# Performance work log

Hardware: AMD Instinct MI355X
Metric: run time of the kernel (lower is better)

## Reference

```python
import jax, jax.numpy as jnp
from jax import lax
import numpy as np

EPS = 1e-5
NEG_SLOPE = 0.2

# 4D conv via lax.conv_general_dilated (supports arbitrary spatial rank)
_DN = ('NCABXY', 'OIABXY', 'NCABXY')  # N,C + 4 spatial dims

def conv4d(x, w):
    # x: (N, Cin, S1, S2, H, W); w: (Cout, Cin, 3, 3, 3, 3); padding=1, stride=1
    return lax.conv_general_dilated(
        x, w,
        window_strides=(1, 1, 1, 1),
        padding=[(1, 1)] * 4,
        dimension_numbers=_DN,
    )

def instance_norm4d(x):
    # normalize per (n, c) over all 4 spatial dims; no affine (PyTorch default)
    mean = jnp.mean(x, axis=(2, 3, 4, 5), keepdims=True)
    var = jnp.var(x, axis=(2, 3, 4, 5), keepdims=True)
    return (x - mean) * lax.rsqrt(var + EPS)

def leaky_relu(x):
    return jnp.where(x >= 0, x, NEG_SLOPE * x)

def setup_inputs() -> dict:
    key = jax.random.key(0)
    k0, k1, k2 = jax.random.split(key, 3)
    image = jax.random.normal(k0, (1, 16, 8, 16, 64, 64), dtype=jnp.float32)
    # He-ish init scale for kernel 3^4
    w1 = jax.random.normal(k1, (32, 16, 3, 3, 3, 3), dtype=jnp.float32) * 0.03
    w2 = jax.random.normal(k2, (32, 32, 3, 3, 3, 3), dtype=jnp.float32) * 0.02
    return {"image": image, "w1": w1, "w2": w2}

def reference(image, w1, w2):
    x = leaky_relu(instance_norm4d(conv4d(image, w1)))
    x = leaky_relu(instance_norm4d(conv4d(x, w2)))
    return x
```

## Files before the change

### kernel.cpp

```cpp
#include <hip/hip_runtime.h>

#define D1 8
#define D2 16
#define HH 64
#define WW 64
#define SPATIAL (D1*D2*HH*WW)
#define EPS 1e-5f
#define NEG 0.2f

typedef unsigned short u16;
typedef __attribute__((ext_vector_type(8))) short s16x8;
typedef __attribute__((ext_vector_type(8))) unsigned short u16x8;
typedef __attribute__((ext_vector_type(4))) unsigned short u16x4;
typedef __attribute__((ext_vector_type(4))) float f32x4;

__device__ __forceinline__ u16 f2bf(float f) {
    unsigned int u = __builtin_bit_cast(unsigned int, f);
    return (u16)((u + 0x7FFFu + ((u >> 16) & 1u)) >> 16);
}
__device__ __forceinline__ float bf2f(u16 u) {
    unsigned int v = ((unsigned int)u) << 16;
    return __builtin_bit_cast(float, v);
}
__device__ __forceinline__ float leaky(float x) {
    return x >= 0.f ? x : NEG * x;
}

__device__ __forceinline__ void decode_block(int flat, int& a, int& b, int& h0) {
    int xcd  = flat & 7;
    int slot = flat >> 3;
    int ht   = slot & 7;
    int b0   = (slot >> 3) & 1;
    a        = (slot >> 4) & 7;
    b        = xcd * 2 + b0;
    h0       = ht * 8;
}

__global__ __launch_bounds__(256)
void prep(const float* __restrict__ img, const float* __restrict__ w1,
          const float* __restrict__ w2, u16* __restrict__ imgT,
          u16* __restrict__ w1t, u16* __restrict__ w2t, float* __restrict__ st)
{
    const int bid = blockIdx.x;
    const int tid = threadIdx.x;
    if (bid < 2048) {
        int p = bid * 256 + tid;
        u16 r[16];
        #pragma unroll
        for (int c = 0; c < 16; ++c)
            r[c] = f2bf(img[(size_t)c * SPATIAL + p]);
        u16x8 lo, hi;
        #pragma unroll
        for (int j = 0; j < 8; ++j) { lo[j] = r[j]; hi[j] = r[8 + j]; }
        u16x8* dst = (u16x8*)(imgT + (size_t)p * 16);
        dst[0] = lo;
        dst[1] = hi;
    } else if (bid < 2264) {
        int i = (bid - 2048) * 256 + tid;
        if (i >= 55296) return;
        int k    = i & 31;
        int co   = (i >> 5) & 31;
        int grp  = (i >> 10) & 1;
        int rest = i >> 11;
        int dh   = rest % 3;
        int p    = rest / 3;
        int da = p / 3, db = p % 3;
        float v = 0.f;
        if (grp == 0) {
            int dw = k >> 4, ci = k & 15;
            v = w1[((((co * 16 + ci) * 3 + da) * 3 + db) * 3 + dh) * 3 + dw];
        } else if (k < 16) {
            v = w1[((((co * 16 + k) * 3 + da) * 3 + db) * 3 + dh) * 3 + 2];
        }
        w1t[i] = f2bf(v);
    } else if (bid < 2588) {
        int i = (bid - 2264) * 256 + tid;
        if (i >= 82944) return;
        int ci = i & 31;
        int co = (i >> 5) & 31;
        int t  = (i >> 10) % 9;
        int p  = (i >> 10) / 9;
        int da = p / 3, db = p % 3, dh = t / 3, dw = t % 3;
        w2t[i] = f2bf(w2[((((co * 32 + ci) * 3 + da) * 3 + db) * 3 + dh) * 3 + dw]);
    } else {
        if (tid < 128) st[tid] = 0.f;
    }
}

#define C1_LDBF(DST, BASE, GRP) { \
    _Pragma("unroll") \
    for (int dh_ = 0; dh_ < 3; ++dh_) { \
        const u16* wb_ = (BASE) + (dh_ * 2 + (GRP)) * 1024; \
        DST[dh_][0] = *(const s16x8*)(wb_ + m * 32 + kq * 8); \
        DST[dh_][1] = *(const s16x8*)(wb_ + (m + 16) * 32 + kq * 8); \
    } }

#define C1_MFMA(BF, CSHIFT) { \
    const int eb_ = (kq & 1) * 8; \
    _Pragma("unroll") \
    for (int x_ = 0; x_ < 10; ++x_) { \
        int pos_ = x_ * 66 + wseg + m + (CSHIFT); \
        s16x8 af_ = *(const s16x8*)&lds[pos_ * 24 + eb_]; \
        _Pragma("unroll") \
        for (int dh_ = 0; dh_ < 3; ++dh_) { \
            int i_ = x_ - dh_; \
            if (i_ >= 0 && i_ < 8) { \
                acc[i_][0] = __builtin_amdgcn_mfma_f32_16x16x32_bf16(af_, BF[dh_][0], acc[i_][0], 0, 0, 0); \
                acc[i_][1] = __builtin_amdgcn_mfma_f32_16x16x32_bf16(af_, BF[dh_][1], acc[i_][1], 0, 0, 0); \
            } \
        } \
    } }

#define C1_PF(K0, K1) { \
    _Pragma("unroll") \
    for (int k_ = (K0); k_ < (K1); ++k_) \
        if ((vmask >> k_) & 1) pf[k_] = *(const u16x8*)(srcn + gbase + k_ * 2048); }

__global__ __launch_bounds__(256, 3)
void conv1_mfma(const u16* __restrict__ xT, const u16* __restrict__ w1t,
                u16* __restrict__ y1, float* __restrict__ st1)
{
    __shared__ __align__(16) u16 lds[660 * 24];
    __shared__ float sred[64];

    const int tid = threadIdx.x;
    int a, b, h0;
    decode_block(blockIdx.x, a, b, h0);
    const int lane = tid & 63;
    const int wv   = tid >> 6;
    const int kq   = lane >> 4;
    const int m    = lane & 15;
    const int wseg = wv << 4;

    unsigned pm = 0;
    #pragma unroll
    for (int p = 0; p < 9; ++p) {
        int ap = a + p / 3 - 1, bp = b + p % 3 - 1;
        if (ap >= 0 && ap < D1 && bp >= 0 && bp < D2) pm |= 1u << p;
    }

    const int p0f  = tid >> 1, g = tid & 1;
    const int hi   = p0f >> 6;
    const int p0c  = p0f & 63;
    unsigned vmask = 0;
    #pragma unroll
    for (int k = 0; k < 5; ++k) {
        int h = h0 - 1 + 2 * k + hi;
        if (h >= 0 && h < HH) vmask |= 1u << k;
    }
    const int gbase = ((h0 - 1 + hi) * WW + p0c) * 16 + g * 8;
    const int lbase = (hi * 66 + p0c + 1) * 24 + g * 8;

    for (int e = tid; e < 660; e += 256) {
        int row = e / 66, col = e - row * 66;
        int h = h0 - 1 + row;
        if (col == 0 || col == 65 || h < 0 || h >= HH) {
            u16x8 z = (u16x8)0;
            *(u16x8*)&lds[e * 24]     = z;
            *(u16x8*)&lds[e * 24 + 8] = z;
        }
    }

    f32x4 acc[8][2];
    #pragma unroll
    for (int i = 0; i < 8; ++i)
        #pragma unroll
        for (int nt = 0; nt < 2; ++nt)
            acc[i][nt] = (f32x4)0.f;

    int p = 0;
    while (!((pm >> p) & 1)) ++p;

    s16x8 bfX[3][2], bfY[3][2];
    C1_LDBF(bfX, w1t + p * 6144, 0);

    u16x8 pf[5];
    {
        const u16* srcn = xT + (size_t)((a + p / 3 - 1) * D2 + (b + p % 3 - 1))
                             * (HH * WW * 16);
        C1_PF(0, 5);
    }

    while (p < 9) {
        int pn = p + 1;
        while (pn < 9 && !((pm >> pn) & 1)) ++pn;

        #pragma unroll
        for (int k = 0; k < 5; ++k)
            if ((vmask >> k) & 1) *(u16x8*)&lds[lbase + k * 3168] = pf[k];
        __syncthreads();

        const u16* srcn = nullptr;
        if (pn < 9)
            srcn = xT + (size_t)((a + pn / 3 - 1) * D2 + (b + pn % 3 - 1))
                      * (HH * WW * 16);

        const u16* wbase = w1t + p * 6144;

        C1_LDBF(bfY, wbase, 1);
        C1_MFMA(bfX, (kq >> 1));
        if (pn < 9) C1_PF(0, 3);

        C1_MFMA(bfY, 2);
        if (pn < 9) C1_PF(3, 5);

        __syncthreads();
        if (pn < 9) C1_LDBF(bfX, w1t + pn * 6144, 0);
        p = pn;
    }

    if (tid < 64) sred[tid] = 0.f;
    __syncthreads();

    float s[2] = {0.f, 0.f}, s2[2] = {0.f, 0.f};
    const size_t plane_out = (size_t)(a * D2 + b) * (HH * WW);
    #pragma unroll
    for (int i = 0; i < 8; ++i) {
        int h  = h0 + i;
        int w0 = wseg + kq * 4;
        #pragma unroll
        for (int nt = 0; nt < 2; ++nt) {
            int co = m + nt * 16;
            #pragma unroll
            for (int reg = 0; reg < 4; ++reg) {
                float v = acc[i][nt][reg];
                s[nt]  += v;
                s2[nt] += v * v;
                y1[(plane_out + h * WW + (w0 + reg)) * 32 + co] = f2bf(v);
            }
        }
    }
    #pragma unroll
    for (int nt = 0; nt < 2; ++nt) {
        s[nt]  += __shfl_xor(s[nt], 16);  s[nt]  += __shfl_xor(s[nt], 32);
        s2[nt] += __shfl_xor(s2[nt], 16); s2[nt] += __shfl_xor(s2[nt], 32);
    }
    if (kq == 0) {
        atomicAdd(&sred[m * 2],            s[0]);
        atomicAdd(&sred[m * 2 + 1],        s2[0]);
        atomicAdd(&sred[(m + 16) * 2],     s[1]);
        atomicAdd(&sred[(m + 16) * 2 + 1], s2[1]);
    }
    __syncthreads();
    if (tid < 64) atomicAdd(&st1[tid], sred[tid]);
}

__global__ __launch_bounds__(256)
void norm1_kernel(u16* __restrict__ y1, const float* __restrict__ st1)
{
    const int tid = threadIdx.x;
    const int q   = tid & 3;
    const float invN = 1.f / (float)SPATIAL;
    float mean[8], scl[8];
    #pragma unroll
    for (int j = 0; j < 8; ++j) {
        int ci  = q * 8 + j;
        float mu = st1[ci * 2] * invN;
        float va = st1[ci * 2 + 1] * invN - mu * mu;
        mean[j] = mu;
        scl[j]  = rsqrtf(va + EPS);
    }
    #pragma unroll
    for (int j4 = 0; j4 < 4; ++j4) {
        size_t gidx = (size_t)blockIdx.x * 1024 + j4 * 256 + tid;
        u16x8* ptr = (u16x8*)(y1 + gidx * 8);
        u16x8 v = *ptr;
        u16x8 o;
        #pragma unroll
        for (int j = 0; j < 8; ++j)
            o[j] = f2bf(leaky((bf2f(v[j]) - mean[j]) * scl[j]));
        *ptr = o;
    }
}

#define C2_LDBF(DST, BASE, DW) { \
    _Pragma("unroll") \
    for (int dh_ = 0; dh_ < 3; ++dh_) { \
        const u16* wb_ = (BASE) + (dh_ * 3 + (DW)) * 1024; \
        DST[dh_][0] = *(const s16x8*)(wb_ + m * 32 + kq * 8); \
        DST[dh_][1] = *(const s16x8*)(wb_ + (m + 16) * 32 + kq * 8); \
    } }

#define C2_MFMA(BF, DW) { \
    _Pragma("unroll") \
    for (int x_ = 0; x_ < 10; ++x_) { \
        int pos_ = x_ * 66 + wseg + (DW) + m; \
        s16x8 af_ = *(const s16x8*)&lds[pos_ * 40 + kq * 8]; \
        _Pragma("unroll") \
        for (int dh_ = 0; dh_ < 3; ++dh_) { \
            int i_ = x_ - dh_; \
            if (i_ >= 0 && i_ < 8) { \
                acc[i_][0] = __builtin_amdgcn_mfma_f32_16x16x32_bf16(af_, BF[dh_][0], acc[i_][0], 0, 0, 0); \
                acc[i_][1] = __builtin_amdgcn_mfma_f32_16x16x32_bf16(af_, BF[dh_][1], acc[i_][1], 0, 0, 0); \
            } \
        } \
    } }

#define C2_PF(K0, K1) { \
    _Pragma("unroll") \
    for (int k_ = (K0); k_ < (K1); ++k_) \
        if ((vmask >> k_) & 1) pf[k_] = *(const u16x8*)(srcn + gbase + k_ * 2048); }

__global__ __launch_bounds__(256, 3)
void conv2_mfma(const u16* __restrict__ y1, const u16* __restrict__ w2t,
                u16* __restrict__ y2, float* __restrict__ st2)
{
    __shared__ __align__(16) u16 lds[660 * 40];
    __shared__ float sred[64];

    const int tid = threadIdx.x;
    int a, b, h0;
    decode_block(blockIdx.x, a, b, h0);
    const int lane = tid & 63;
    const int wv   = tid >> 6;
    const int kq   = lane >> 4;
    const int m    = lane & 15;
    const int wseg = wv << 4;

    unsigned pm = 0;
    #pragma unroll
    for (int p = 0; p < 9; ++p) {
        int ap = a + p / 3 - 1, bp = b + p % 3 - 1;
        if (ap >= 0 && ap < D1 && bp >= 0 && bp < D2) pm |= 1u << p;
    }

    const int p0 = tid >> 2, q = tid & 3;
    unsigned vmask = 0;
    #pragma unroll
    for (int k = 0; k < 10; ++k) {
        int h = h0 - 1 + k;
        if (h >= 0 && h < HH) vmask |= 1u << k;
    }
    const int gbase = ((h0 - 1) * WW + p0) * 32 + q * 8;
    const int lbase = (p0 + 1) * 40 + q * 8;

    for (int e = tid; e < 660; e += 256) {
        int row = e / 66, col = e - row * 66;
        int h = h0 - 1 + row;
        if (col == 0 || col == 65 || h < 0 || h >= HH) {
            u16x8 z = (u16x8)0;
            #pragma unroll
            for (int gg = 0; gg < 4; ++gg)
                *(u16x8*)&lds[e * 40 + gg * 8] = z;
        }
    }

    f32x4 acc[8][2];
    #pragma unroll
    for (int i = 0; i < 8; ++i)
        #pragma unroll
        for (int nt = 0; nt < 2; ++nt)
            acc[i][nt] = (f32x4)0.f;

    int p = 0;
    while (!((pm >> p) & 1)) ++p;

    s16x8 bfX[3][2], bfY[3][2];
    C2_LDBF(bfX, w2t + p * 9216, 0);

    u16x8 pf[10];
    {
        const u16* srcn = y1 + (size_t)((a + p / 3 - 1) * D2 + (b + p % 3 - 1))
                             * (HH * WW * 32);
        C2_PF(0, 10);
    }

    while (p < 9) {
        int pn = p + 1;
        while (pn < 9 && !((pm >> pn) & 1)) ++pn;

        #pragma unroll
        for (int k = 0; k < 10; ++k)
            if ((vmask >> k) & 1) *(u16x8*)&lds[lbase + k * 2640] = pf[k];
        __syncthreads();

        const u16* srcn = nullptr;
        if (pn < 9)
            srcn = y1 + (size_t)((a + pn / 3 - 1) * D2 + (b + pn % 3 - 1))
                      * (HH * WW * 32);

        const u16* wbase = w2t + p * 9216;

        C2_LDBF(bfY, wbase, 1);
        C2_MFMA(bfX, 0);
        if (pn < 9) C2_PF(0, 4);

        C2_LDBF(bfX, wbase, 2);
        C2_MFMA(bfY, 1);
        if (pn < 9) C2_PF(4, 7);

        C2_MFMA(bfX, 2);
        if (pn < 9) C2_PF(7, 10);

        __syncthreads();
        if (pn < 9) C2_LDBF(bfX, w2t + pn * 9216, 0);
        p = pn;
    }

    if (tid < 64) sred[tid] = 0.f;
    __syncthreads();

    float s[2] = {0.f, 0.f}, s2[2] = {0.f, 0.f};
    #pragma unroll
    for (int i = 0; i < 8; ++i) {
        int h  = h0 + i;
        int w0 = wseg + kq * 4;
        #pragma unroll
        for (int nt = 0; nt < 2; ++nt) {
            int co = m + nt * 16;
            u16x4 pk;
            #pragma unroll
            for (int reg = 0; reg < 4; ++reg) {
                float v = acc[i][nt][reg];
                s[nt]  += v;
                s2[nt] += v * v;
                pk[reg] = f2bf(v);
            }
            size_t off = ((size_t)(co * D1 + a) * D2 + b) * (HH * WW) + h * WW + w0;
            *(u16x4*)(y2 + off) = pk;
        }
    }
    #pragma unroll
    for (int nt = 0; nt < 2; ++nt) {
        s[nt]  += __shfl_xor(s[nt], 16);  s[nt]  += __shfl_xor(s[nt], 32);
        s2[nt] += __shfl_xor(s2[nt], 16); s2[nt] += __shfl_xor(s2[nt], 32);
    }
    if (kq == 0) {
        atomicAdd(&sred[m * 2],            s[0]);
        atomicAdd(&sred[m * 2 + 1],        s2[0]);
        atomicAdd(&sred[(m + 16) * 2],     s[1]);
        atomicAdd(&sred[(m + 16) * 2 + 1], s2[1]);
    }
    __syncthreads();
    if (tid < 64) atomicAdd(&st2[tid], sred[tid]);
}

__global__ __launch_bounds__(256)
void norm2_kernel(const u16* __restrict__ y2, const float* __restrict__ st2,
                  float* __restrict__ out)
{
    size_t i8 = (size_t)blockIdx.x * 256 + threadIdx.x;
    int c = (int)(i8 >> 16);
    const float invN = 1.f / (float)SPATIAL;
    float mu = st2[c * 2] * invN;
    float va = st2[c * 2 + 1] * invN - mu * mu;
    float sc = rsqrtf(va + EPS);
    u16x8 v = *(const u16x8*)(y2 + i8 * 8);
    float4 o0, o1;
    o0.x = leaky((bf2f(v[0]) - mu) * sc);
    o0.y = leaky((bf2f(v[1]) - mu) * sc);
    o0.z = leaky((bf2f(v[2]) - mu) * sc);
    o0.w = leaky((bf2f(v[3]) - mu) * sc);
    o1.x = leaky((bf2f(v[4]) - mu) * sc);
    o1.y = leaky((bf2f(v[5]) - mu) * sc);
    o1.z = leaky((bf2f(v[6]) - mu) * sc);
    o1.w = leaky((bf2f(v[7]) - mu) * sc);
    float4* dst = (float4*)(out + i8 * 8);
    dst[0] = o0;
    dst[1] = o1;
}

extern "C" void kernel_launch(void* const* d_in, const int* in_sizes, int n_in,
                              void* d_out, int out_size, void* d_ws, size_t ws_size,
                              hipStream_t stream)
{
    const float* image = (const float*)d_in[0];
    const float* w1    = (const float*)d_in[1];
    const float* w2    = (const float*)d_in[2];
    float* out = (float*)d_out;

    u16*   imgT = (u16*)d_ws;
    u16*   y1   = (u16*)((char*)d_ws + 33554432);
    u16*   y2   = imgT;
    float* st   = (float*)((char*)d_ws + 67108864);
    float* st1  = st;
    float* st2  = st + 64;

    u16* w1t = (u16*)((char*)d_out + 66832384);
    u16* w2t = (u16*)((char*)d_out + 66942976);

    prep<<<2589, 256, 0, stream>>>(image, w1, w2, imgT, w1t, w2t, st);

    conv1_mfma<<<1024, 256, 0, stream>>>(imgT, w1t, y1, st1);
    norm1_kernel<<<2048, 256, 0, stream>>>(y1, st1);
    conv2_mfma<<<1024, 256, 0, stream>>>(y1, w2t, y2, st2);
    norm2_kernel<<<8192, 256, 0, stream>>>(y2, st2, out);
}
```

Before: 249.9 us.

## Split output channels across waves with 512-thread conv blocks

Both conv kernels now launch 512 threads per block. The 8 waves are split into 4 width segments times 2 output-channel halves, so each wave accumulates a single 16-channel tile instead of two. This halves per-thread accumulator, weight-fragment and prefetch registers, and the global-to-LDS staging work is spread over twice as many threads. The intent is more resident waves per CU to hide latency. The cost is that every A fragment is now read from LDS by two waves, which doubles LDS read traffic, and each block synchronizes more threads.

```diff
diff --git a/kernel.cpp b/kernel.cpp
--- a/kernel.cpp
+++ b/kernel.cpp
@@ -91,8 +91,7 @@
     _Pragma("unroll") \
     for (int dh_ = 0; dh_ < 3; ++dh_) { \
         const u16* wb_ = (BASE) + (dh_ * 2 + (GRP)) * 1024; \
-        DST[dh_][0] = *(const s16x8*)(wb_ + m * 32 + kq * 8); \
-        DST[dh_][1] = *(const s16x8*)(wb_ + (m + 16) * 32 + kq * 8); \
+        DST[dh_] = *(const s16x8*)(wb_ + cow * 32 + kq * 8); \
     } }
 
 #define C1_MFMA(BF, CSHIFT) { \
@@ -104,19 +103,17 @@
         _Pragma("unroll") \
         for (int dh_ = 0; dh_ < 3; ++dh_) { \
             int i_ = x_ - dh_; \
-            if (i_ >= 0 && i_ < 8) { \
-                acc[i_][0] = __builtin_amdgcn_mfma_f32_16x16x32_bf16(af_, BF[dh_][0], acc[i_][0], 0, 0, 0); \
-                acc[i_][1] = __builtin_amdgcn_mfma_f32_16x16x32_bf16(af_, BF[dh_][1], acc[i_][1], 0, 0, 0); \
-            } \
+            if (i_ >= 0 && i_ < 8) \
+                acc[i_] = __builtin_amdgcn_mfma_f32_16x16x32_bf16(af_, BF[dh_], acc[i_], 0, 0, 0); \
         } \
     } }
 
 #define C1_PF(K0, K1) { \
     _Pragma("unroll") \
     for (int k_ = (K0); k_ < (K1); ++k_) \
-        if ((vmask >> k_) & 1) pf[k_] = *(const u16x8*)(srcn + gbase + k_ * 2048); }
-
-__global__ __launch_bounds__(256, 3)
+        if ((vmask >> k_) & 1) pf[k_] = *(const u16x8*)(srcn + gbase + k_ * 4096); }
+
+__global__ __launch_bounds__(512, 4)
 void conv1_mfma(const u16* __restrict__ xT, const u16* __restrict__ w1t,
                 u16* __restrict__ y1, float* __restrict__ st1)
 {
@@ -130,7 +127,8 @@
     const int wv   = tid >> 6;
     const int kq   = lane >> 4;
     const int m    = lane & 15;
-    const int wseg = wv << 4;
+    const int wseg = (wv & 3) << 4;
+    const int cow  = m + (wv >> 2) * 16;
 
     unsigned pm = 0;
     #pragma unroll
@@ -139,46 +137,43 @@
         if (ap >= 0 && ap < D1 && bp >= 0 && bp < D2) pm |= 1u << p;
     }
 
-    const int p0f  = tid >> 1, g = tid & 1;
-    const int hi   = p0f >> 6;
-    const int p0c  = p0f & 63;
+    const int g = tid & 1, cr = tid >> 1;
+    const int col = cr & 63, rq = cr >> 6;
     unsigned vmask = 0;
     #pragma unroll
-    for (int k = 0; k < 5; ++k) {
-        int h = h0 - 1 + 2 * k + hi;
-        if (h >= 0 && h < HH) vmask |= 1u << k;
-    }
-    const int gbase = ((h0 - 1 + hi) * WW + p0c) * 16 + g * 8;
-    const int lbase = (hi * 66 + p0c + 1) * 24 + g * 8;
-
-    for (int e = tid; e < 660; e += 256) {
-        int row = e / 66, col = e - row * 66;
+    for (int k = 0; k < 3; ++k) {
+        int row = rq + 4 * k;
         int h = h0 - 1 + row;
-        if (col == 0 || col == 65 || h < 0 || h >= HH) {
+        if (row < 10 && h >= 0 && h < HH) vmask |= 1u << k;
+    }
+    const int gbase = ((h0 - 1 + rq) * WW + col) * 16 + g * 8;
+    const int lbase = (rq * 66 + col + 1) * 24 + g * 8;
+
+    for (int e = tid; e < 660; e += 512) {
+        int row = e / 66, c2 = e - row * 66;
+        int h = h0 - 1 + row;
+        if (c2 == 0 || c2 == 65 || h < 0 || h >= HH) {
             u16x8 z = (u16x8)0;
             *(u16x8*)&lds[e * 24]     = z;
             *(u16x8*)&lds[e * 24 + 8] = z;
         }
     }
 
-    f32x4 acc[8][2];
-    #pragma unroll
-    for (int i = 0; i < 8; ++i)
-        #pragma unroll
-        for (int nt = 0; nt < 2; ++nt)
-            acc[i][nt] = (f32x4)0.f;
+    f32x4 acc[8];
+    #pragma unroll
+    for (int i = 0; i < 8; ++i) acc[i] = (f32x4)0.f;
 
     int p = 0;
     while (!((pm >> p) & 1)) ++p;
 
-    s16x8 bfX[3][2], bfY[3][2];
+    s16x8 bfX[3], bfY[3];
     C1_LDBF(bfX, w1t + p * 6144, 0);
 
-    u16x8 pf[5];
+    u16x8 pf[3];
     {
         const u16* srcn = xT + (size_t)((a + p / 3 - 1) * D2 + (b + p % 3 - 1))
                              * (HH * WW * 16);
-        C1_PF(0, 5);
+        C1_PF(0, 3);
     }
 
     while (p < 9) {
@@ -186,8 +181,8 @@
         while (pn < 9 && !((pm >> pn) & 1)) ++pn;
 
         #pragma unroll
-        for (int k = 0; k < 5; ++k)
-            if ((vmask >> k) & 1) *(u16x8*)&lds[lbase + k * 3168] = pf[k];
+        for (int k = 0; k < 3; ++k)
+            if ((vmask >> k) & 1) *(u16x8*)&lds[lbase + k * 6336] = pf[k];
         __syncthreads();
 
         const u16* srcn = nullptr;
@@ -199,10 +194,10 @@
 
         C1_LDBF(bfY, wbase, 1);
         C1_MFMA(bfX, (kq >> 1));
-        if (pn < 9) C1_PF(0, 3);
+        if (pn < 9) C1_PF(0, 2);
 
         C1_MFMA(bfY, 2);
-        if (pn < 9) C1_PF(3, 5);
+        if (pn < 9) C1_PF(2, 3);
 
         __syncthreads();
         if (pn < 9) C1_LDBF(bfX, w1t + pn * 6144, 0);
@@ -212,34 +207,25 @@
     if (tid < 64) sred[tid] = 0.f;
     __syncthreads();
 
-    float s[2] = {0.f, 0.f}, s2[2] = {0.f, 0.f};
+    float s = 0.f, s2v = 0.f;
     const size_t plane_out = (size_t)(a * D2 + b) * (HH * WW);
     #pragma unroll
     for (int i = 0; i < 8; ++i) {
         int h  = h0 + i;
         int w0 = wseg + kq * 4;
         #pragma unroll
-        for (int nt = 0; nt < 2; ++nt) {
-            int co = m + nt * 16;
-            #pragma unroll
-            for (int reg = 0; reg < 4; ++reg) {
-                float v = acc[i][nt][reg];
-                s[nt]  += v;
-                s2[nt] += v * v;
-                y1[(plane_out + h * WW + (w0 + reg)) * 32 + co] = f2bf(v);
-            }
+        for (int reg = 0; reg < 4; ++reg) {
+            float v = acc[i][reg];
+            s  += v;
+            s2v += v * v;
+            y1[(plane_out + h * WW + (w0 + reg)) * 32 + cow] = f2bf(v);
         }
     }
-    #pragma unroll
-    for (int nt = 0; nt < 2; ++nt) {
-        s[nt]  += __shfl_xor(s[nt], 16);  s[nt]  += __shfl_xor(s[nt], 32);
-        s2[nt] += __shfl_xor(s2[nt], 16); s2[nt] += __shfl_xor(s2[nt], 32);
-    }
+    s   += __shfl_xor(s, 16);   s   += __shfl_xor(s, 32);
+    s2v += __shfl_xor(s2v, 16); s2v += __shfl_xor(s2v, 32);
     if (kq == 0) {
-        atomicAdd(&sred[m * 2],            s[0]);
-        atomicAdd(&sred[m * 2 + 1],        s2[0]);
-        atomicAdd(&sred[(m + 16) * 2],     s[1]);
-        atomicAdd(&sred[(m + 16) * 2 + 1], s2[1]);
+        atomicAdd(&sred[cow * 2],     s);
+        atomicAdd(&sred[cow * 2 + 1], s2v);
     }
     __syncthreads();
     if (tid < 64) atomicAdd(&st1[tid], sred[tid]);
@@ -277,8 +263,7 @@
     _Pragma("unroll") \
     for (int dh_ = 0; dh_ < 3; ++dh_) { \
         const u16* wb_ = (BASE) + (dh_ * 3 + (DW)) * 1024; \
-        DST[dh_][0] = *(const s16x8*)(wb_ + m * 32 + kq * 8); \
-        DST[dh_][1] = *(const s16x8*)(wb_ + (m + 16) * 32 + kq * 8); \
+        DST[dh_] = *(const s16x8*)(wb_ + cow * 32 + kq * 8); \
     } }
 
 #define C2_MFMA(BF, DW) { \
@@ -289,19 +274,17 @@
         _Pragma("unroll") \
         for (int dh_ = 0; dh_ < 3; ++dh_) { \
             int i_ = x_ - dh_; \
-            if (i_ >= 0 && i_ < 8) { \
-                acc[i_][0] = __builtin_amdgcn_mfma_f32_16x16x32_bf16(af_, BF[dh_][0], acc[i_][0], 0, 0, 0); \
-                acc[i_][1] = __builtin_amdgcn_mfma_f32_16x16x32_bf16(af_, BF[dh_][1], acc[i_][1], 0, 0, 0); \
-            } \
+            if (i_ >= 0 && i_ < 8) \
+                acc[i_] = __builtin_amdgcn_mfma_f32_16x16x32_bf16(af_, BF[dh_], acc[i_], 0, 0, 0); \
         } \
     } }
 
 #define C2_PF(K0, K1) { \
     _Pragma("unroll") \
     for (int k_ = (K0); k_ < (K1); ++k_) \
-        if ((vmask >> k_) & 1) pf[k_] = *(const u16x8*)(srcn + gbase + k_ * 2048); }
-
-__global__ __launch_bounds__(256, 3)
+        if ((vmask >> k_) & 1) pf[k_] = *(const u16x8*)(srcn + gbase + k_ * 4096); }
+
+__global__ __launch_bounds__(512, 4)
 void conv2_mfma(const u16* __restrict__ y1, const u16* __restrict__ w2t,
                 u16* __restrict__ y2, float* __restrict__ st2)
 {
@@ -315,7 +298,8 @@
     const int wv   = tid >> 6;
     const int kq   = lane >> 4;
     const int m    = lane & 15;
-    const int wseg = wv << 4;
+    const int wseg = (wv & 3) << 4;
+    const int cow  = m + (wv >> 2) * 16;
 
     unsigned pm = 0;
     #pragma unroll
@@ -324,20 +308,21 @@
         if (ap >= 0 && ap < D1 && bp >= 0 && bp < D2) pm |= 1u << p;
     }
 
-    const int p0 = tid >> 2, q = tid & 3;
+    const int q = tid & 3, cr = tid >> 2;
+    const int col = cr & 63, rh = cr >> 6;
     unsigned vmask = 0;
     #pragma unroll
-    for (int k = 0; k < 10; ++k) {
-        int h = h0 - 1 + k;
+    for (int k = 0; k < 5; ++k) {
+        int h = h0 - 1 + rh + 2 * k;
         if (h >= 0 && h < HH) vmask |= 1u << k;
     }
-    const int gbase = ((h0 - 1) * WW + p0) * 32 + q * 8;
-    const int lbase = (p0 + 1) * 40 + q * 8;
-
-    for (int e = tid; e < 660; e += 256) {
-        int row = e / 66, col = e - row * 66;
+    const int gbase = ((h0 - 1 + rh) * WW + col) * 32 + q * 8;
+    const int lbase = (rh * 66 + col + 1) * 40 + q * 8;
+
+    for (int e = tid; e < 660; e += 512) {
+        int row = e / 66, c2 = e - row * 66;
         int h = h0 - 1 + row;
-        if (col == 0 || col == 65 || h < 0 || h >= HH) {
+        if (c2 == 0 || c2 == 65 || h < 0 || h >= HH) {
             u16x8 z = (u16x8)0;
             #pragma unroll
             for (int gg = 0; gg < 4; ++gg)
@@ -345,24 +330,21 @@
         }
     }
 
-    f32x4 acc[8][2];
-    #pragma unroll
-    for (int i = 0; i < 8; ++i)
-        #pragma unroll
-        for (int nt = 0; nt < 2; ++nt)
-            acc[i][nt] = (f32x4)0.f;
+    f32x4 acc[8];
+    #pragma unroll
+    for (int i = 0; i < 8; ++i) acc[i] = (f32x4)0.f;
 
     int p = 0;
     while (!((pm >> p) & 1)) ++p;
 
-    s16x8 bfX[3][2], bfY[3][2];
+    s16x8 bfX[3], bfY[3];
     C2_LDBF(bfX, w2t + p * 9216, 0);
 
-    u16x8 pf[10];
+    u16x8 pf[5];
     {
         const u16* srcn = y1 + (size_t)((a + p / 3 - 1) * D2 + (b + p % 3 - 1))
                              * (HH * WW * 32);
-        C2_PF(0, 10);
+        C2_PF(0, 5);
     }
 
     while (p < 9) {
@@ -370,8 +352,8 @@
         while (pn < 9 && !((pm >> pn) & 1)) ++pn;
 
         #pragma unroll
-        for (int k = 0; k < 10; ++k)
-            if ((vmask >> k) & 1) *(u16x8*)&lds[lbase + k * 2640] = pf[k];
+        for (int k = 0; k < 5; ++k)
+            if ((vmask >> k) & 1) *(u16x8*)&lds[lbase + k * 5280] = pf[k];
         __syncthreads();
 
         const u16* srcn = nullptr;
@@ -383,14 +365,14 @@
 
         C2_LDBF(bfY, wbase, 1);
         C2_MFMA(bfX, 0);
-        if (pn < 9) C2_PF(0, 4);
+        if (pn < 9) C2_PF(0, 2);
 
         C2_LDBF(bfX, wbase, 2);
         C2_MFMA(bfY, 1);
-        if (pn < 9) C2_PF(4, 7);
+        if (pn < 9) C2_PF(2, 4);
 
         C2_MFMA(bfX, 2);
-        if (pn < 9) C2_PF(7, 10);
+        if (pn < 9) C2_PF(4, 5);
 
         __syncthreads();
         if (pn < 9) C2_LDBF(bfX, w2t + pn * 9216, 0);
@@ -400,36 +382,27 @@
     if (tid < 64) sred[tid] = 0.f;
     __syncthreads();
 
-    float s[2] = {0.f, 0.f}, s2[2] = {0.f, 0.f};
+    float s = 0.f, s2v = 0.f;
     #pragma unroll
     for (int i = 0; i < 8; ++i) {
         int h  = h0 + i;
         int w0 = wseg + kq * 4;
-        #pragma unroll
-        for (int nt = 0; nt < 2; ++nt) {
-            int co = m + nt * 16;
-            u16x4 pk;
-            #pragma unroll
-            for (int reg = 0; reg < 4; ++reg) {
-                float v = acc[i][nt][reg];
-                s[nt]  += v;
-                s2[nt] += v * v;
-                pk[reg] = f2bf(v);
-            }
-            size_t off = ((size_t)(co * D1 + a) * D2 + b) * (HH * WW) + h * WW + w0;
-            *(u16x4*)(y2 + off) = pk;
+        u16x4 pk;
+        #pragma unroll
+        for (int reg = 0; reg < 4; ++reg) {
+            float v = acc[i][reg];
+            s  += v;
+            s2v += v * v;
+            pk[reg] = f2bf(v);
         }
-    }
-    #pragma unroll
-    for (int nt = 0; nt < 2; ++nt) {
-        s[nt]  += __shfl_xor(s[nt], 16);  s[nt]  += __shfl_xor(s[nt], 32);
-        s2[nt] += __shfl_xor(s2[nt], 16); s2[nt] += __shfl_xor(s2[nt], 32);
-    }
+        size_t off = ((size_t)(cow * D1 + a) * D2 + b) * (HH * WW) + h * WW + w0;
+        *(u16x4*)(y2 + off) = pk;
+    }
+    s   += __shfl_xor(s, 16);   s   += __shfl_xor(s, 32);
+    s2v += __shfl_xor(s2v, 16); s2v += __shfl_xor(s2v, 32);
     if (kq == 0) {
-        atomicAdd(&sred[m * 2],            s[0]);
-        atomicAdd(&sred[m * 2 + 1],        s2[0]);
-        atomicAdd(&sred[(m + 16) * 2],     s[1]);
-        atomicAdd(&sred[(m + 16) * 2 + 1], s2[1]);
+        atomicAdd(&sred[cow * 2],     s);
+        atomicAdd(&sred[cow * 2 + 1], s2v);
     }
     __syncthreads();
     if (tid < 64) atomicAdd(&st2[tid], sred[tid]);
@@ -481,8 +454,8 @@
 
     prep<<<2589, 256, 0, stream>>>(image, w1, w2, imgT, w1t, w2t, st);
 
-    conv1_mfma<<<1024, 256, 0, stream>>>(imgT, w1t, y1, st1);
+    conv1_mfma<<<1024, 512, 0, stream>>>(imgT, w1t, y1, st1);
     norm1_kernel<<<2048, 256, 0, stream>>>(y1, st1);
-    conv2_mfma<<<1024, 256, 0, stream>>>(y1, w2t, y2, st2);
+    conv2_mfma<<<1024, 512, 0, stream>>>(y1, w2t, y2, st2);
     norm2_kernel<<<8192, 256, 0, stream>>>(y2, st2, out);
 }
```

Result: no change. 249.4 us (-0.2%).

## Split conv2 output channels across twice as many waves per block

Applied to the files above, without the earlier changes.

conv2 now launches 512 threads per block. Each group of four waves covers one 16-channel half of the 32 output channels, so each wave keeps 8 accumulators instead of 16 and loads one weight fragment per tap instead of two. The cooperative LDS fill is spread over 512 threads with 5 prefetch registers each. The aim is lower register pressure and more waves in flight to hide MFMA and memory latency, at the cost of every wave re-reading the same activation fragments from LDS.

```diff
diff --git a/kernel.cpp b/kernel.cpp
--- a/kernel.cpp
+++ b/kernel.cpp
@@ -277,8 +277,7 @@
     _Pragma("unroll") \
     for (int dh_ = 0; dh_ < 3; ++dh_) { \
         const u16* wb_ = (BASE) + (dh_ * 3 + (DW)) * 1024; \
-        DST[dh_][0] = *(const s16x8*)(wb_ + m * 32 + kq * 8); \
-        DST[dh_][1] = *(const s16x8*)(wb_ + (m + 16) * 32 + kq * 8); \
+        DST[dh_] = *(const s16x8*)(wb_ + cow * 32 + kq * 8); \
     } }
 
 #define C2_MFMA(BF, DW) { \
@@ -289,19 +288,17 @@
         _Pragma("unroll") \
         for (int dh_ = 0; dh_ < 3; ++dh_) { \
             int i_ = x_ - dh_; \
-            if (i_ >= 0 && i_ < 8) { \
-                acc[i_][0] = __builtin_amdgcn_mfma_f32_16x16x32_bf16(af_, BF[dh_][0], acc[i_][0], 0, 0, 0); \
-                acc[i_][1] = __builtin_amdgcn_mfma_f32_16x16x32_bf16(af_, BF[dh_][1], acc[i_][1], 0, 0, 0); \
-            } \
+            if (i_ >= 0 && i_ < 8) \
+                acc[i_] = __builtin_amdgcn_mfma_f32_16x16x32_bf16(af_, BF[dh_], acc[i_], 0, 0, 0); \
         } \
     } }
 
 #define C2_PF(K0, K1) { \
     _Pragma("unroll") \
     for (int k_ = (K0); k_ < (K1); ++k_) \
-        if ((vmask >> k_) & 1) pf[k_] = *(const u16x8*)(srcn + gbase + k_ * 2048); }
-
-__global__ __launch_bounds__(256, 3)
+        if ((vmask >> k_) & 1) pf[k_] = *(const u16x8*)(srcn + gbase + k_ * 4096); }
+
+__global__ __launch_bounds__(512, 4)
 void conv2_mfma(const u16* __restrict__ y1, const u16* __restrict__ w2t,
                 u16* __restrict__ y2, float* __restrict__ st2)
 {
@@ -315,7 +312,8 @@
     const int wv   = tid >> 6;
     const int kq   = lane >> 4;
     const int m    = lane & 15;
-    const int wseg = wv << 4;
+    const int wseg = (wv & 3) << 4;
+    const int cow  = m + (wv >> 2) * 16;
 
     unsigned pm = 0;
     #pragma unroll
@@ -324,20 +322,21 @@
         if (ap >= 0 && ap < D1 && bp >= 0 && bp < D2) pm |= 1u << p;
     }
 
-    const int p0 = tid >> 2, q = tid & 3;
+    const int q = tid & 3, cr = tid >> 2;
+    const int col = cr & 63, rh = cr >> 6;
     unsigned vmask = 0;
     #pragma unroll
-    for (int k = 0; k < 10; ++k) {
-        int h = h0 - 1 + k;
+    for (int k = 0; k < 5; ++k) {
+        int h = h0 - 1 + rh + 2 * k;
         if (h >= 0 && h < HH) vmask |= 1u << k;
     }
-    const int gbase = ((h0 - 1) * WW + p0) * 32 + q * 8;
-    const int lbase = (p0 + 1) * 40 + q * 8;
-
-    for (int e = tid; e < 660; e += 256) {
-        int row = e / 66, col = e - row * 66;
+    const int gbase = ((h0 - 1 + rh) * WW + col) * 32 + q * 8;
+    const int lbase = (rh * 66 + col + 1) * 40 + q * 8;
+
+    for (int e = tid; e < 660; e += 512) {
+        int row = e / 66, c2 = e - row * 66;
         int h = h0 - 1 + row;
-        if (col == 0 || col == 65 || h < 0 || h >= HH) {
+        if (c2 == 0 || c2 == 65 || h < 0 || h >= HH) {
             u16x8 z = (u16x8)0;
             #pragma unroll
             for (int gg = 0; gg < 4; ++gg)
@@ -345,24 +344,21 @@
         }
     }
 
-    f32x4 acc[8][2];
-    #pragma unroll
-    for (int i = 0; i < 8; ++i)
-        #pragma unroll
-        for (int nt = 0; nt < 2; ++nt)
-            acc[i][nt] = (f32x4)0.f;
+    f32x4 acc[8];
+    #pragma unroll
+    for (int i = 0; i < 8; ++i) acc[i] = (f32x4)0.f;
 
     int p = 0;
     while (!((pm >> p) & 1)) ++p;
 
-    s16x8 bfX[3][2], bfY[3][2];
+    s16x8 bfX[3], bfY[3];
     C2_LDBF(bfX, w2t + p * 9216, 0);
 
-    u16x8 pf[10];
+    u16x8 pf[5];
     {
         const u16* srcn = y1 + (size_t)((a + p / 3 - 1) * D2 + (b + p % 3 - 1))
                              * (HH * WW * 32);
-        C2_PF(0, 10);
+        C2_PF(0, 5);
     }
 
     while (p < 9) {
@@ -370,8 +366,8 @@
         while (pn < 9 && !((pm >> pn) & 1)) ++pn;
 
         #pragma unroll
-        for (int k = 0; k < 10; ++k)
-            if ((vmask >> k) & 1) *(u16x8*)&lds[lbase + k * 2640] = pf[k];
+        for (int k = 0; k < 5; ++k)
+            if ((vmask >> k) & 1) *(u16x8*)&lds[lbase + k * 5280] = pf[k];
         __syncthreads();
 
         const u16* srcn = nullptr;
@@ -383,14 +379,14 @@
 
         C2_LDBF(bfY, wbase, 1);
         C2_MFMA(bfX, 0);
-        if (pn < 9) C2_PF(0, 4);
+        if (pn < 9) C2_PF(0, 2);
 
         C2_LDBF(bfX, wbase, 2);
         C2_MFMA(bfY, 1);
-        if (pn < 9) C2_PF(4, 7);
+        if (pn < 9) C2_PF(2, 4);
 
         C2_MFMA(bfX, 2);
-        if (pn < 9) C2_PF(7, 10);
+        if (pn < 9) C2_PF(4, 5);
 
         __syncthreads();
         if (pn < 9) C2_LDBF(bfX, w2t + pn * 9216, 0);
@@ -400,36 +396,27 @@
     if (tid < 64) sred[tid] = 0.f;
     __syncthreads();
 
-    float s[2] = {0.f, 0.f}, s2[2] = {0.f, 0.f};
+    float s = 0.f, s2v = 0.f;
     #pragma unroll
     for (int i = 0; i < 8; ++i) {
         int h  = h0 + i;
         int w0 = wseg + kq * 4;
-        #pragma unroll
-        for (int nt = 0; nt < 2; ++nt) {
-            int co = m + nt * 16;
-            u16x4 pk;
-            #pragma unroll
-            for (int reg = 0; reg < 4; ++reg) {
-                float v = acc[i][nt][reg];
-                s[nt]  += v;
-                s2[nt] += v * v;
-                pk[reg] = f2bf(v);
-            }
-            size_t off = ((size_t)(co * D1 + a) * D2 + b) * (HH * WW) + h * WW + w0;
-            *(u16x4*)(y2 + off) = pk;
+        u16x4 pk;
+        #pragma unroll
+        for (int reg = 0; reg < 4; ++reg) {
+            float v = acc[i][reg];
+            s  += v;
+            s2v += v * v;
+            pk[reg] = f2bf(v);
         }
-    }
-    #pragma unroll
-    for (int nt = 0; nt < 2; ++nt) {
-        s[nt]  += __shfl_xor(s[nt], 16);  s[nt]  += __shfl_xor(s[nt], 32);
-        s2[nt] += __shfl_xor(s2[nt], 16); s2[nt] += __shfl_xor(s2[nt], 32);
-    }
+        size_t off = ((size_t)(cow * D1 + a) * D2 + b) * (HH * WW) + h * WW + w0;
+        *(u16x4*)(y2 + off) = pk;
+    }
+    s   += __shfl_xor(s, 16);   s   += __shfl_xor(s, 32);
+    s2v += __shfl_xor(s2v, 16); s2v += __shfl_xor(s2v, 32);
     if (kq == 0) {
-        atomicAdd(&sred[m * 2],            s[0]);
-        atomicAdd(&sred[m * 2 + 1],        s2[0]);
-        atomicAdd(&sred[(m + 16) * 2],     s[1]);
-        atomicAdd(&sred[(m + 16) * 2 + 1], s2[1]);
+        atomicAdd(&sred[cow * 2],     s);
+        atomicAdd(&sred[cow * 2 + 1], s2v);
     }
     __syncthreads();
     if (tid < 64) atomicAdd(&st2[tid], sred[tid]);
@@ -483,6 +470,6 @@
 
     conv1_mfma<<<1024, 256, 0, stream>>>(imgT, w1t, y1, st1);
     norm1_kernel<<<2048, 256, 0, stream>>>(y1, st1);
-    conv2_mfma<<<1024, 256, 0, stream>>>(y1, w2t, y2, st2);
+    conv2_mfma<<<1024, 512, 0, stream>>>(y1, w2t, y2, st2);
     norm2_kernel<<<8192, 256, 0, stream>>>(y2, st2, out);
 }
```

Result: no change. 252.2 us (+0.9%).
